# Kernel tuning notes

Hardware: AMD Instinct MI355X
Metric: run time of the kernel (lower is better)

Reference implementation:

```python
import jax, jax.numpy as jnp
import numpy as np

N_NODES = 100000
N_EDGES = 640000
D = 128
N_LAYERS = 4
N_GRAPHS = 512


def setup_inputs() -> dict:
    key = jax.random.key(0)
    ks = jax.random.split(key, 12)
    x = jax.random.normal(ks[0], (N_NODES, D), dtype=jnp.float32)
    edge_index = jax.random.randint(ks[1], (2, N_EDGES), 0, N_NODES, dtype=jnp.int64)
    batch = jnp.sort(jax.random.randint(ks[2], (N_NODES,), 0, N_GRAPHS, dtype=jnp.int64))
    s = 1.0 / np.sqrt(D)
    convW = jax.random.uniform(ks[3], (N_LAYERS, D, D), jnp.float32, -s, s)
    convB = jax.random.uniform(ks[4], (N_LAYERS, D), jnp.float32, -s, s)
    W1 = jax.random.uniform(ks[5], (D, D), jnp.float32, -s, s)
    b1 = jax.random.uniform(ks[6], (D,), jnp.float32, -s, s)
    W2 = jax.random.uniform(ks[7], (D, D), jnp.float32, -s, s)
    b2 = jax.random.uniform(ks[8], (D,), jnp.float32, -s, s)
    W3 = jax.random.uniform(ks[9], (D, 1), jnp.float32, -s, s)
    b3 = jax.random.uniform(ks[10], (1,), jnp.float32, -s, s)
    return {"x": x, "edge_index": edge_index, "batch": batch,
            "convW": convW, "convB": convB,
            "W1": W1, "b1": b1, "W2": W2, "b2": b2, "W3": W3, "b3": b3}


def reference(x, edge_index, batch, convW, convB, W1, b1, W2, b2, W3, b3):
    N = x.shape[0]
    # GCNConv default: add self-loops, symmetric deg^-1/2 normalization
    loops = jnp.arange(N, dtype=edge_index.dtype)
    src = jnp.concatenate([edge_index[0], loops])  # [E+N]
    dst = jnp.concatenate([edge_index[1], loops])
    deg = jax.ops.segment_sum(jnp.ones_like(dst, dtype=x.dtype), dst, num_segments=N)
    dinv = jnp.where(deg > 0, jax.lax.rsqrt(deg), 0.0)
    norm = (dinv[src] * dinv[dst])[:, None]  # [E+N, 1]
    h = x
    for i in range(N_LAYERS):
        hw = h @ convW[i]                                   # [N, D]
        msg = hw[src] * norm                                # gather + scale [E+N, D]
        agg = jax.ops.segment_sum(msg, dst, num_segments=N)  # scatter-add [N, D]
        h = jax.nn.relu(agg + convB[i])
    pooled = jax.ops.segment_sum(h, batch, num_segments=N_GRAPHS)  # [G, D]
    z = jax.nn.relu(pooled @ W1 + b1)
    z = jax.nn.relu(z @ W2 + b2)
    return jax.nn.sigmoid(z @ W3 + b3)  # [G, 1]
```

## Files before the change

kernel.cpp:

```cpp
#include <hip/hip_runtime.h>
#include <math.h>

#define D 128
#define LSTRIDE 136

typedef _Float16 half8 __attribute__((ext_vector_type(8)));
typedef _Float16 half4v __attribute__((ext_vector_type(4)));
typedef _Float16 half2v __attribute__((ext_vector_type(2)));
typedef float f32x4 __attribute__((ext_vector_type(4)));


__global__ void k_count(const int* __restrict__ ei, int* __restrict__ counts,
                        int* __restrict__ pidx, int E) {
    int e0 = (blockIdx.x * blockDim.x + threadIdx.x) * 4;
    if (e0 + 3 < E) {
        int4 d4 = *(const int4*)(ei + E + e0);
        int4 p;
        p.x = atomicAdd(&counts[d4.x], 1);
        p.y = atomicAdd(&counts[d4.y], 1);
        p.z = atomicAdd(&counts[d4.z], 1);
        p.w = atomicAdd(&counts[d4.w], 1);
        *(int4*)(pidx + e0) = p;
    } else {
        for (int e = e0; e < E; e++) pidx[e] = atomicAdd(&counts[ei[E + e]], 1);
    }
}

__global__ __launch_bounds__(256) void k_scan1(const int* __restrict__ counts,
                                               int* __restrict__ rowptr,
                                               int* __restrict__ bsums,
                                               float* __restrict__ dinv, int N) {
    __shared__ int sh[256];
    const int t = threadIdx.x;
    const int base = blockIdx.x * 1024 + t * 4;
    int c[4];
#pragma unroll
    for (int j = 0; j < 4; j++) c[j] = (base + j < N) ? counts[base + j] : 0;
#pragma unroll
    for (int j = 0; j < 4; j++)
        if (base + j < N) dinv[base + j] = rsqrtf((float)(c[j] + 1));
    int tsum = c[0] + c[1] + c[2] + c[3];
    sh[t] = tsum;
    __syncthreads();
    for (int off = 1; off < 256; off <<= 1) {
        int v = (t >= off) ? sh[t - off] : 0;
        __syncthreads();
        sh[t] += v;
        __syncthreads();
    }
    int run = (t == 0) ? 0 : sh[t - 1];
    if (t == 255) bsums[blockIdx.x] = sh[255];
#pragma unroll
    for (int j = 0; j < 4; j++) {
        if (base + j <= N) rowptr[base + j] = run;
        run += c[j];
    }
}

__global__ __launch_bounds__(256) void k_scan3(int* __restrict__ rowptr,
                                               const int* __restrict__ bsums,
                                               int NB, int N) {
    __shared__ int pre[128];
    const int t = threadIdx.x;
    if (t < 128) pre[t] = (t < NB) ? bsums[t] : 0;
    __syncthreads();
    for (int off = 1; off < 128; off <<= 1) {
        int v = (t >= off && t < 128) ? pre[t - off] : 0;
        __syncthreads();
        if (t < 128) pre[t] += v;
        __syncthreads();
    }
    int i = blockIdx.x * blockDim.x + t;
    if (i <= N) {
        int b = i >> 10;
        rowptr[i] += (b == 0) ? 0 : pre[b - 1];
    }
}

__global__ void k_fill(const int* __restrict__ ei, const int* __restrict__ rowptr,
                       const int* __restrict__ pidx, int* __restrict__ srcs, int E) {
    int e0 = (blockIdx.x * blockDim.x + threadIdx.x) * 4;
    if (e0 + 3 < E) {
        int4 s4 = *(const int4*)(ei + e0);
        int4 d4 = *(const int4*)(ei + E + e0);
        int4 p4 = *(const int4*)(pidx + e0);
        int r0 = rowptr[d4.x], r1 = rowptr[d4.y], r2 = rowptr[d4.z], r3 = rowptr[d4.w];
        srcs[r0 + p4.x] = s4.x;
        srcs[r1 + p4.y] = s4.y;
        srcs[r2 + p4.z] = s4.z;
        srcs[r3 + p4.w] = s4.w;
    } else {
        for (int e = e0; e < E; e++)
            srcs[rowptr[ei[E + e]] + pidx[e]] = ei[e];
    }
}


__global__ void k_cvt(const float* __restrict__ x, const float* __restrict__ dinv,
                      _Float16* __restrict__ y, int n8) {
    int i = blockIdx.x * blockDim.x + threadIdx.x;
    if (i >= n8) return;
    float s = dinv[i >> 4];
    const float4 v0 = *(const float4*)(x + (size_t)i * 8);
    const float4 v1 = *(const float4*)(x + (size_t)i * 8 + 4);
    half8 h;
    h[0] = (_Float16)(v0.x * s); h[1] = (_Float16)(v0.y * s);
    h[2] = (_Float16)(v0.z * s); h[3] = (_Float16)(v0.w * s);
    h[4] = (_Float16)(v1.x * s); h[5] = (_Float16)(v1.y * s);
    h[6] = (_Float16)(v1.z * s); h[7] = (_Float16)(v1.w * s);
    *(half8*)(y + (size_t)i * 8) = h;
}


__global__ __launch_bounds__(256) void k_prepw(const float* __restrict__ convW,
                                               _Float16* __restrict__ Wf) {
    const int l = blockIdx.x >> 3;
    const int slot = (blockIdx.x & 7) * 256 + threadIdx.x;
    const float* W = convW + (size_t)l * D * D;
    const int p = slot >> 6, ln = slot & 63;
    const int s = p >> 3, c = p & 7;
    const int kbase = s * 32 + ((ln >> 4) << 3);
    const int n = (c << 4) + (ln & 15);
    half8 hv;
#pragma unroll
    for (int j = 0; j < 8; j++) hv[j] = (_Float16)W[(size_t)(kbase + j) * D + n];
    *(half8*)(Wf + (size_t)l * D * D + (size_t)slot * 8) = hv;
}


__global__ __launch_bounds__(512) void k_layer(
        const _Float16* __restrict__ gin,
        const int* __restrict__ rowptr, const int* __restrict__ srcs,
        const float* __restrict__ dinv,
        const _Float16* __restrict__ Wf,
        const float* __restrict__ bias,
        _Float16* __restrict__ gout, int N, int last) {
    __shared__ _Float16 S[128 * LSTRIDE];

    const int tid  = threadIdx.x;
    const int w    = tid >> 6;
    const int lane = tid & 63;
    const int q    = lane >> 4;
    const int l16  = lane & 15;
    const int nb0  = blockIdx.x * 128;

    const int cb = l16 * 8;
    for (int it = 0; it < 4; ++it) {
        const int nl = w * 16 + q * 4 + it;
        const int node = nb0 + nl;
        float a[8];
#pragma unroll
        for (int j = 0; j < 8; j++) a[j] = 0.f;

        if (node < N) {
            half8 sv = *(const half8*)(gin + (size_t)node * D + cb);
#pragma unroll
            for (int j = 0; j < 8; j++) a[j] = (float)sv[j];
            const int beg = rowptr[node];
            const int end = rowptr[node + 1];
            int e = beg;
            for (; e + 3 < end; e += 4) {
                int s0 = srcs[e], s1 = srcs[e + 1], s2 = srcs[e + 2], s3 = srcs[e + 3];
                half8 v0 = *(const half8*)(gin + (size_t)s0 * D + cb);
                half8 v1 = *(const half8*)(gin + (size_t)s1 * D + cb);
                half8 v2 = *(const half8*)(gin + (size_t)s2 * D + cb);
                half8 v3 = *(const half8*)(gin + (size_t)s3 * D + cb);
#pragma unroll
                for (int j = 0; j < 8; j++)
                    a[j] += ((float)v0[j] + (float)v1[j]) + ((float)v2[j] + (float)v3[j]);
            }
            for (; e < end; e++) {
                int s0 = srcs[e];
                half8 v0 = *(const half8*)(gin + (size_t)s0 * D + cb);
#pragma unroll
                for (int j = 0; j < 8; j++) a[j] += (float)v0[j];
            }
        }
        const float sc = (node < N) ? dinv[node] : 0.f;
        half8 o;
#pragma unroll
        for (int j = 0; j < 8; j++) o[j] = (_Float16)(a[j] * sc);
        *(half8*)(&S[nl * LSTRIDE + cb]) = o;
    }
    __syncthreads();

    f32x4 acc[8];
#pragma unroll
    for (int cc = 0; cc < 8; cc++) acc[cc] = (f32x4){0.f, 0.f, 0.f, 0.f};

    const int nl = w * 16 + l16;
#pragma unroll
    for (int s = 0; s < 4; s++) {
        half8 bf = *(const half8*)(&S[nl * LSTRIDE + s * 32 + q * 8]);
#pragma unroll
        for (int cc = 0; cc < 8; cc++) {
            half8 wh = *(const half8*)(Wf + (size_t)((s * 8 + cc) * 64 + lane) * 8);
            acc[cc] = __builtin_amdgcn_mfma_f32_16x16x32_f16(wh, bf, acc[cc], 0, 0, 0);
        }
    }

    const int node = nb0 + nl;
    if (node < N) {
        const float scale = last ? 1.0f : dinv[node];
        _Float16* rp = gout + (size_t)node * D + q * 4;
#pragma unroll
        for (int cc = 0; cc < 8; cc++) {
            const float4 bc = *(const float4*)(bias + cc * 16 + q * 4);
            half4v o;
            o[0] = (_Float16)(fmaxf(acc[cc][0] + bc.x, 0.f) * scale);
            o[1] = (_Float16)(fmaxf(acc[cc][1] + bc.y, 0.f) * scale);
            o[2] = (_Float16)(fmaxf(acc[cc][2] + bc.z, 0.f) * scale);
            o[3] = (_Float16)(fmaxf(acc[cc][3] + bc.w, 0.f) * scale);
            *(half4v*)(rp + cc * 16) = o;
        }
    }
}


__global__ __launch_bounds__(256) void k_poolhead(
        const _Float16* __restrict__ h, const int* __restrict__ batch,
        const float* __restrict__ W1, const float* __restrict__ b1,
        const float* __restrict__ W2, const float* __restrict__ b2,
        const float* __restrict__ W3, const float* __restrict__ b3,
        float* __restrict__ out, int N) {
    __shared__ int sb[2];
    __shared__ float part[4][D];
    __shared__ float v[D];
    __shared__ float z[D];
    __shared__ float red[D];

    const int g = blockIdx.x;
    const int t = threadIdx.x;

    if (t < 2) {
        int target = g + t;
        int lo = 0, hi = N;
        while (lo < hi) {
            int mid = (lo + hi) >> 1;
            if (batch[mid] < target) lo = mid + 1; else hi = mid;
        }
        sb[t] = lo;
    }
    __syncthreads();
    const int rs = sb[0], re = sb[1];

    const int w = t >> 6;
    const int lane = t & 63;
    const int c = lane * 2;

    float ax = 0.f, ay = 0.f;
    for (int r = rs + w; r < re; r += 4) {
        half2v vv = *(const half2v*)(h + (size_t)r * D + c);
        ax += (float)vv[0]; ay += (float)vv[1];
    }
    part[w][c] = ax;
    part[w][c + 1] = ay;
    __syncthreads();

    if (t < D) v[t] = part[0][t] + part[1][t] + part[2][t] + part[3][t];
    __syncthreads();

    if (t < D) {
        float s = b1[t];
        for (int k = 0; k < D; k++) s = fmaf(v[k], W1[(size_t)k * D + t], s);
        z[t] = fmaxf(s, 0.f);
    }
    __syncthreads();

    if (t < D) {
        float s = b2[t];
        for (int k = 0; k < D; k++) s = fmaf(z[k], W2[(size_t)k * D + t], s);
        red[t] = fmaxf(s, 0.f) * W3[t];
    }
    __syncthreads();
    for (int off = 64; off >= 1; off >>= 1) {
        if (t < off) red[t] += red[t + off];
        __syncthreads();
    }
    if (t == 0) out[g] = 1.f / (1.f + expf(-(red[0] + b3[0])));
}


extern "C" void kernel_launch(void* const* d_in, const int* in_sizes, int n_in,
                              void* d_out, int out_size, void* d_ws, size_t ws_size,
                              hipStream_t stream) {
    const float* x     = (const float*)d_in[0];
    const int*   ei    = (const int*)d_in[1];
    const int*   batch = (const int*)d_in[2];
    const float* convW = (const float*)d_in[3];
    const float* convB = (const float*)d_in[4];
    const float* W1 = (const float*)d_in[5];
    const float* b1 = (const float*)d_in[6];
    const float* W2 = (const float*)d_in[7];
    const float* b2 = (const float*)d_in[8];
    const float* W3 = (const float*)d_in[9];
    const float* b3 = (const float*)d_in[10];
    float* out = (float*)d_out;

    const int N = in_sizes[0] / D;
    const int E = in_sizes[1] / 2;
    const int G = out_size;
    const int NB = (N + 1023) / 1024;

    char* w = (char*)d_ws;
    size_t off = 0;
    auto alloc = [&](size_t bytes) -> char* {
        char* p = w + off;
        off += (bytes + 255) & ~(size_t)255;
        return p;
    };
    float*     dinv   = (float*)alloc((size_t)N * 4);
    _Float16*  gA     = (_Float16*)alloc((size_t)N * D * 2);
    _Float16*  gB     = (_Float16*)alloc((size_t)N * D * 2);
    _Float16*  Wf     = (_Float16*)alloc((size_t)4 * D * D * 2);
    int*       counts = (int*)alloc((size_t)N * 4);
    int*       rowptr = (int*)alloc((size_t)(N + 1) * 4);
    int*       pidx   = (int*)alloc((size_t)E * 4);
    int*       srcs   = (int*)alloc((size_t)E * 4);
    int*       bsums  = (int*)alloc((size_t)NB * 4);

    hipMemsetAsync(counts, 0, (size_t)N * 4, stream);
    k_count<<<(E / 4 + 255) / 256, 256, 0, stream>>>(ei, counts, pidx, E);
    k_prepw<<<32, 256, 0, stream>>>(convW, Wf);
    k_scan1<<<NB, 256, 0, stream>>>(counts, rowptr, bsums, dinv, N);
    k_cvt<<<(N * D / 8 + 255) / 256, 256, 0, stream>>>(x, dinv, gA, N * D / 8);
    k_scan3<<<(N + 1 + 255) / 256, 256, 0, stream>>>(rowptr, bsums, NB, N);
    k_fill<<<(E / 4 + 255) / 256, 256, 0, stream>>>(ei, rowptr, pidx, srcs, E);

    const int layer_grid = (N + 127) / 128;
    const _Float16* gi = gA;
    _Float16* go = gB;
    for (int l = 0; l < 4; l++) {
        k_layer<<<layer_grid, 512, 0, stream>>>(gi, rowptr, srcs, dinv,
                                                Wf + (size_t)l * D * D,
                                                convB + (size_t)l * D,
                                                go, N, l == 3);
        const _Float16* tmp = go;
        go = (_Float16*)gi;
        gi = tmp;
    }

    k_poolhead<<<G, 256, 0, stream>>>(gi, batch, W1, b1, W2, b2, W3, b3, out, N);
}
```

Before: 360.5 us.

## Store intermediate node features in FP8 and fuse setup kernels

Intermediate per-layer node features are now stored as FP8 (e4m3) rather than FP16, which halves the bytes moved by the random neighbor gathers that dominate each GCN layer. The last layer still writes FP16 for pooling. Count and weight-prep kernels are merged into one launch, and the scan fixup is merged with the input conversion, to cut launch overhead. FP8 storage reduces precision of the aggregated features and may threaten tolerance.

```diff
diff --git a/kernel.cpp b/kernel.cpp
--- a/kernel.cpp
+++ b/kernel.cpp
@@ -8,21 +8,48 @@
 typedef _Float16 half4v __attribute__((ext_vector_type(4)));
 typedef _Float16 half2v __attribute__((ext_vector_type(2)));
 typedef float f32x4 __attribute__((ext_vector_type(4)));
-
-
-__global__ void k_count(const int* __restrict__ ei, int* __restrict__ counts,
-                        int* __restrict__ pidx, int E) {
-    int e0 = (blockIdx.x * blockDim.x + threadIdx.x) * 4;
-    if (e0 + 3 < E) {
-        int4 d4 = *(const int4*)(ei + E + e0);
-        int4 p;
-        p.x = atomicAdd(&counts[d4.x], 1);
-        p.y = atomicAdd(&counts[d4.y], 1);
-        p.z = atomicAdd(&counts[d4.z], 1);
-        p.w = atomicAdd(&counts[d4.w], 1);
-        *(int4*)(pidx + e0) = p;
+typedef float f32x2 __attribute__((ext_vector_type(2)));
+typedef unsigned char uchar;
+
+__device__ __forceinline__ void acc_fp8x8(float* a, uint2 u) {
+    f32x2 p0 = __builtin_amdgcn_cvt_pk_f32_fp8((int)u.x, false);
+    f32x2 p1 = __builtin_amdgcn_cvt_pk_f32_fp8((int)u.x, true);
+    f32x2 p2 = __builtin_amdgcn_cvt_pk_f32_fp8((int)u.y, false);
+    f32x2 p3 = __builtin_amdgcn_cvt_pk_f32_fp8((int)u.y, true);
+    a[0] += p0[0]; a[1] += p0[1]; a[2] += p1[0]; a[3] += p1[1];
+    a[4] += p2[0]; a[5] += p2[1]; a[6] += p3[0]; a[7] += p3[1];
+}
+
+
+__global__ void k_fat1(const int* __restrict__ ei, int* __restrict__ counts,
+                       int* __restrict__ pidx, int E, int countBlocks,
+                       const float* __restrict__ convW, _Float16* __restrict__ Wf) {
+    if ((int)blockIdx.x < countBlocks) {
+        int e0 = (blockIdx.x * blockDim.x + threadIdx.x) * 4;
+        if (e0 + 3 < E) {
+            int4 d4 = *(const int4*)(ei + E + e0);
+            int4 p;
+            p.x = atomicAdd(&counts[d4.x], 1);
+            p.y = atomicAdd(&counts[d4.y], 1);
+            p.z = atomicAdd(&counts[d4.z], 1);
+            p.w = atomicAdd(&counts[d4.w], 1);
+            *(int4*)(pidx + e0) = p;
+        } else {
+            for (int e = e0; e < E; e++) pidx[e] = atomicAdd(&counts[ei[E + e]], 1);
+        }
     } else {
-        for (int e = e0; e < E; e++) pidx[e] = atomicAdd(&counts[ei[E + e]], 1);
+        const int bid = blockIdx.x - countBlocks;
+        const int l = bid >> 3;
+        const int slot = (bid & 7) * 256 + threadIdx.x;
+        const float* W = convW + (size_t)l * D * D;
+        const int p = slot >> 6, ln = slot & 63;
+        const int s = p >> 3, c = p & 7;
+        const int kbase = s * 32 + ((ln >> 4) << 3);
+        const int n = (c << 4) + (ln & 15);
+        half8 hv;
+#pragma unroll
+        for (int j = 0; j < 8; j++) hv[j] = (_Float16)W[(size_t)(kbase + j) * D + n];
+        *(half8*)(Wf + (size_t)l * D * D + (size_t)slot * 8) = hv;
     }
 }
 
@@ -57,23 +84,41 @@
     }
 }
 
-__global__ __launch_bounds__(256) void k_scan3(int* __restrict__ rowptr,
-                                               const int* __restrict__ bsums,
-                                               int NB, int N) {
-    __shared__ int pre[128];
-    const int t = threadIdx.x;
-    if (t < 128) pre[t] = (t < NB) ? bsums[t] : 0;
-    __syncthreads();
-    for (int off = 1; off < 128; off <<= 1) {
-        int v = (t >= off && t < 128) ? pre[t - off] : 0;
+
+__global__ __launch_bounds__(256) void k_fat2(int* __restrict__ rowptr,
+                                              const int* __restrict__ bsums,
+                                              int NB, int N, int scanBlocks,
+                                              const float* __restrict__ x,
+                                              const float* __restrict__ dinv,
+                                              uchar* __restrict__ g8) {
+    if ((int)blockIdx.x < scanBlocks) {
+        __shared__ int pre[128];
+        const int t = threadIdx.x;
+        if (t < 128) pre[t] = (t < NB) ? bsums[t] : 0;
         __syncthreads();
-        if (t < 128) pre[t] += v;
-        __syncthreads();
-    }
-    int i = blockIdx.x * blockDim.x + t;
-    if (i <= N) {
-        int b = i >> 10;
-        rowptr[i] += (b == 0) ? 0 : pre[b - 1];
+        for (int off = 1; off < 128; off <<= 1) {
+            int v = (t >= off && t < 128) ? pre[t - off] : 0;
+            __syncthreads();
+            if (t < 128) pre[t] += v;
+            __syncthreads();
+        }
+        int i = blockIdx.x * blockDim.x + t;
+        if (i <= N) {
+            int b = i >> 10;
+            rowptr[i] += (b == 0) ? 0 : pre[b - 1];
+        }
+    } else {
+        int i = (blockIdx.x - scanBlocks) * blockDim.x + threadIdx.x;
+        const int n8 = N * (D / 8);
+        if (i >= n8) return;
+        float s = dinv[i >> 4];
+        const float4 v0 = *(const float4*)(x + (size_t)i * 8);
+        const float4 v1 = *(const float4*)(x + (size_t)i * 8 + 4);
+        int lo = __builtin_amdgcn_cvt_pk_fp8_f32(v0.x * s, v0.y * s, 0, false);
+        lo     = __builtin_amdgcn_cvt_pk_fp8_f32(v0.z * s, v0.w * s, lo, true);
+        int hi = __builtin_amdgcn_cvt_pk_fp8_f32(v1.x * s, v1.y * s, 0, false);
+        hi     = __builtin_amdgcn_cvt_pk_fp8_f32(v1.z * s, v1.w * s, hi, true);
+        *(int2*)(g8 + (size_t)i * 8) = make_int2(lo, hi);
     }
 }
 
@@ -96,45 +141,14 @@
 }
 
 
-__global__ void k_cvt(const float* __restrict__ x, const float* __restrict__ dinv,
-                      _Float16* __restrict__ y, int n8) {
-    int i = blockIdx.x * blockDim.x + threadIdx.x;
-    if (i >= n8) return;
-    float s = dinv[i >> 4];
-    const float4 v0 = *(const float4*)(x + (size_t)i * 8);
-    const float4 v1 = *(const float4*)(x + (size_t)i * 8 + 4);
-    half8 h;
-    h[0] = (_Float16)(v0.x * s); h[1] = (_Float16)(v0.y * s);
-    h[2] = (_Float16)(v0.z * s); h[3] = (_Float16)(v0.w * s);
-    h[4] = (_Float16)(v1.x * s); h[5] = (_Float16)(v1.y * s);
-    h[6] = (_Float16)(v1.z * s); h[7] = (_Float16)(v1.w * s);
-    *(half8*)(y + (size_t)i * 8) = h;
-}
-
-
-__global__ __launch_bounds__(256) void k_prepw(const float* __restrict__ convW,
-                                               _Float16* __restrict__ Wf) {
-    const int l = blockIdx.x >> 3;
-    const int slot = (blockIdx.x & 7) * 256 + threadIdx.x;
-    const float* W = convW + (size_t)l * D * D;
-    const int p = slot >> 6, ln = slot & 63;
-    const int s = p >> 3, c = p & 7;
-    const int kbase = s * 32 + ((ln >> 4) << 3);
-    const int n = (c << 4) + (ln & 15);
-    half8 hv;
-#pragma unroll
-    for (int j = 0; j < 8; j++) hv[j] = (_Float16)W[(size_t)(kbase + j) * D + n];
-    *(half8*)(Wf + (size_t)l * D * D + (size_t)slot * 8) = hv;
-}
-
-
 __global__ __launch_bounds__(512) void k_layer(
-        const _Float16* __restrict__ gin,
+        const uchar* __restrict__ g8in,
         const int* __restrict__ rowptr, const int* __restrict__ srcs,
         const float* __restrict__ dinv,
         const _Float16* __restrict__ Wf,
         const float* __restrict__ bias,
-        _Float16* __restrict__ gout, int N, int last) {
+        uchar* __restrict__ g8out, _Float16* __restrict__ g16out,
+        int N, int last) {
     __shared__ _Float16 S[128 * LSTRIDE];
 
     const int tid  = threadIdx.x;
@@ -143,8 +157,8 @@
     const int q    = lane >> 4;
     const int l16  = lane & 15;
     const int nb0  = blockIdx.x * 128;
-
-    const int cb = l16 * 8;
+    const int cb   = l16 * 8;
+
     for (int it = 0; it < 4; ++it) {
         const int nl = w * 16 + q * 4 + it;
         const int node = nb0 + nl;
@@ -153,27 +167,24 @@
         for (int j = 0; j < 8; j++) a[j] = 0.f;
 
         if (node < N) {
-            half8 sv = *(const half8*)(gin + (size_t)node * D + cb);
-#pragma unroll
-            for (int j = 0; j < 8; j++) a[j] = (float)sv[j];
+            acc_fp8x8(a, *(const uint2*)(g8in + (size_t)node * D + cb));
             const int beg = rowptr[node];
             const int end = rowptr[node + 1];
             int e = beg;
             for (; e + 3 < end; e += 4) {
                 int s0 = srcs[e], s1 = srcs[e + 1], s2 = srcs[e + 2], s3 = srcs[e + 3];
-                half8 v0 = *(const half8*)(gin + (size_t)s0 * D + cb);
-                half8 v1 = *(const half8*)(gin + (size_t)s1 * D + cb);
-                half8 v2 = *(const half8*)(gin + (size_t)s2 * D + cb);
-                half8 v3 = *(const half8*)(gin + (size_t)s3 * D + cb);
-#pragma unroll
-                for (int j = 0; j < 8; j++)
-                    a[j] += ((float)v0[j] + (float)v1[j]) + ((float)v2[j] + (float)v3[j]);
+                uint2 u0 = *(const uint2*)(g8in + (size_t)s0 * D + cb);
+                uint2 u1 = *(const uint2*)(g8in + (size_t)s1 * D + cb);
+                uint2 u2 = *(const uint2*)(g8in + (size_t)s2 * D + cb);
+                uint2 u3 = *(const uint2*)(g8in + (size_t)s3 * D + cb);
+                acc_fp8x8(a, u0);
+                acc_fp8x8(a, u1);
+                acc_fp8x8(a, u2);
+                acc_fp8x8(a, u3);
             }
             for (; e < end; e++) {
-                int s0 = srcs[e];
-                half8 v0 = *(const half8*)(gin + (size_t)s0 * D + cb);
-#pragma unroll
-                for (int j = 0; j < 8; j++) a[j] += (float)v0[j];
+                uint2 u0 = *(const uint2*)(g8in + (size_t)srcs[e] * D + cb);
+                acc_fp8x8(a, u0);
             }
         }
         const float sc = (node < N) ? dinv[node] : 0.f;
@@ -201,17 +212,32 @@
 
     const int node = nb0 + nl;
     if (node < N) {
-        const float scale = last ? 1.0f : dinv[node];
-        _Float16* rp = gout + (size_t)node * D + q * 4;
-#pragma unroll
-        for (int cc = 0; cc < 8; cc++) {
-            const float4 bc = *(const float4*)(bias + cc * 16 + q * 4);
-            half4v o;
-            o[0] = (_Float16)(fmaxf(acc[cc][0] + bc.x, 0.f) * scale);
-            o[1] = (_Float16)(fmaxf(acc[cc][1] + bc.y, 0.f) * scale);
-            o[2] = (_Float16)(fmaxf(acc[cc][2] + bc.z, 0.f) * scale);
-            o[3] = (_Float16)(fmaxf(acc[cc][3] + bc.w, 0.f) * scale);
-            *(half4v*)(rp + cc * 16) = o;
+        if (last) {
+            _Float16* rp = g16out + (size_t)node * D + q * 4;
+#pragma unroll
+            for (int cc = 0; cc < 8; cc++) {
+                const float4 bc = *(const float4*)(bias + cc * 16 + q * 4);
+                half4v o;
+                o[0] = (_Float16)fmaxf(acc[cc][0] + bc.x, 0.f);
+                o[1] = (_Float16)fmaxf(acc[cc][1] + bc.y, 0.f);
+                o[2] = (_Float16)fmaxf(acc[cc][2] + bc.z, 0.f);
+                o[3] = (_Float16)fmaxf(acc[cc][3] + bc.w, 0.f);
+                *(half4v*)(rp + cc * 16) = o;
+            }
+        } else {
+            const float scale = dinv[node];
+            uchar* rp = g8out + (size_t)node * D + q * 4;
+#pragma unroll
+            for (int cc = 0; cc < 8; cc++) {
+                const float4 bc = *(const float4*)(bias + cc * 16 + q * 4);
+                float o0 = fmaxf(acc[cc][0] + bc.x, 0.f) * scale;
+                float o1 = fmaxf(acc[cc][1] + bc.y, 0.f) * scale;
+                float o2 = fmaxf(acc[cc][2] + bc.z, 0.f) * scale;
+                float o3 = fmaxf(acc[cc][3] + bc.w, 0.f) * scale;
+                int pk = __builtin_amdgcn_cvt_pk_fp8_f32(o0, o1, 0, false);
+                pk     = __builtin_amdgcn_cvt_pk_fp8_f32(o2, o3, pk, true);
+                *(int*)(rp + cc * 16) = pk;
+            }
         }
     }
 }
@@ -310,8 +336,9 @@
         return p;
     };
     float*     dinv   = (float*)alloc((size_t)N * 4);
-    _Float16*  gA     = (_Float16*)alloc((size_t)N * D * 2);
-    _Float16*  gB     = (_Float16*)alloc((size_t)N * D * 2);
+    uchar*     g8A    = (uchar*)alloc((size_t)N * D);
+    uchar*     g8B    = (uchar*)alloc((size_t)N * D);
+    _Float16*  g16    = (_Float16*)alloc((size_t)N * D * 2);
     _Float16*  Wf     = (_Float16*)alloc((size_t)4 * D * D * 2);
     int*       counts = (int*)alloc((size_t)N * 4);
     int*       rowptr = (int*)alloc((size_t)(N + 1) * 4);
@@ -320,25 +347,28 @@
     int*       bsums  = (int*)alloc((size_t)NB * 4);
 
     hipMemsetAsync(counts, 0, (size_t)N * 4, stream);
-    k_count<<<(E / 4 + 255) / 256, 256, 0, stream>>>(ei, counts, pidx, E);
-    k_prepw<<<32, 256, 0, stream>>>(convW, Wf);
+    const int countBlocks = (E / 4 + 255) / 256;
+    k_fat1<<<countBlocks + 32, 256, 0, stream>>>(ei, counts, pidx, E, countBlocks,
+                                                 convW, Wf);
     k_scan1<<<NB, 256, 0, stream>>>(counts, rowptr, bsums, dinv, N);
-    k_cvt<<<(N * D / 8 + 255) / 256, 256, 0, stream>>>(x, dinv, gA, N * D / 8);
-    k_scan3<<<(N + 1 + 255) / 256, 256, 0, stream>>>(rowptr, bsums, NB, N);
+    const int scanBlocks = (N + 1 + 255) / 256;
+    const int cvtBlocks  = (N * (D / 8) + 255) / 256;
+    k_fat2<<<scanBlocks + cvtBlocks, 256, 0, stream>>>(rowptr, bsums, NB, N, scanBlocks,
+                                                       x, dinv, g8A);
     k_fill<<<(E / 4 + 255) / 256, 256, 0, stream>>>(ei, rowptr, pidx, srcs, E);
 
     const int layer_grid = (N + 127) / 128;
-    const _Float16* gi = gA;
-    _Float16* go = gB;
+    const uchar* gi = g8A;
+    uchar* go = g8B;
     for (int l = 0; l < 4; l++) {
         k_layer<<<layer_grid, 512, 0, stream>>>(gi, rowptr, srcs, dinv,
                                                 Wf + (size_t)l * D * D,
                                                 convB + (size_t)l * D,
-                                                go, N, l == 3);
-        const _Float16* tmp = go;
-        go = (_Float16*)gi;
+                                                go, g16, N, l == 3);
+        const uchar* tmp = go;
+        go = (uchar*)gi;
         gi = tmp;
     }
 
-    k_poolhead<<<G, 256, 0, stream>>>(gi, batch, W1, b1, W2, b2, W3, b3, out, N);
-}
+    k_poolhead<<<G, 256, 0, stream>>>(g16, batch, W1, b1, W2, b2, W3, b3, out, N);
+}
```

After: 377.6 us. +4.7%, slower.
